# Kernel tuning notes

Hardware: AMD Instinct MI355X
Metric: run time of the kernel (lower is better)

The kernel has to match this reference:

```python
import jax, jax.numpy as jnp
import numpy as np

N, M, F0, FB, F, H, NC, NCONV = 60000, 12, 92, 41, 64, 128, 2000, 3
EPS = 1e-5


def setup_inputs() -> dict:
    key = jax.random.key(0)
    ks = jax.random.split(key, 12)
    s = 0.05
    return {
        "atom_fea": jax.random.normal(ks[0], (N, F0), jnp.float32),
        "nbr_fea": jax.random.normal(ks[1], (N, M, FB), jnp.float32),
        "nbr_fea_idx": jax.random.randint(ks[2], (N, M), 0, N),
        "crystal_atom_idx": jnp.sort(jax.random.randint(ks[3], (N,), 0, NC)),
        "W_emb": jax.random.normal(ks[4], (F0, F), jnp.float32) * s,
        "b_emb": jnp.zeros((F,), jnp.float32),
        "W_full": jax.random.normal(ks[5], (NCONV, 2 * F + FB, 2 * F), jnp.float32) * s,
        "b_full": jnp.zeros((NCONV, 2 * F), jnp.float32),
        "g1": jnp.ones((NCONV, 2 * F), jnp.float32),
        "be1": jnp.zeros((NCONV, 2 * F), jnp.float32),
        "g2": jnp.ones((NCONV, F), jnp.float32),
        "be2": jnp.zeros((NCONV, F), jnp.float32),
        "W_fc": jax.random.normal(ks[6], (F, H), jnp.float32) * s,
        "b_fc": jnp.zeros((H,), jnp.float32),
        "W_out": jax.random.normal(ks[7], (H, 1), jnp.float32) * s,
        "b_out": jnp.zeros((1,), jnp.float32),
    }


def _bn(x, g, b):
    # training-mode batch norm over leading (row) dim
    m = x.mean(axis=0)
    v = x.var(axis=0)
    return (x - m) * jax.lax.rsqrt(v + EPS) * g + b


def _conv_layer(x, nbr_fea, nbr_fea_idx, Wf, bf, g1, be1, g2, be2):
    n, m = nbr_fea_idx.shape
    f = x.shape[1]
    atom_nbr = x[nbr_fea_idx]  # (N, M, F) gather
    total = jnp.concatenate(
        [jnp.broadcast_to(x[:, None, :], (n, m, f)), atom_nbr, nbr_fea], axis=2
    )  # (N, M, 2F+FB)
    gated = total @ Wf + bf  # (N, M, 2F)
    gated = _bn(gated.reshape(-1, 2 * f), g1, be1).reshape(n, m, 2 * f)
    nbr_filter, nbr_core = jnp.split(gated, 2, axis=2)
    summed = jnp.sum(jax.nn.sigmoid(nbr_filter) * jax.nn.softplus(nbr_core), axis=1)
    summed = _bn(summed, g2, be2)
    return jax.nn.softplus(x + summed)


def reference(atom_fea, nbr_fea, nbr_fea_idx, crystal_atom_idx, W_emb, b_emb,
              W_full, b_full, g1, be1, g2, be2, W_fc, b_fc, W_out, b_out):
    x = atom_fea @ W_emb + b_emb  # (N, F)
    for i in range(NCONV):
        x = _conv_layer(x, nbr_fea, nbr_fea_idx, W_full[i], b_full[i],
                        g1[i], be1[i], g2[i], be2[i])
    # mean-pool atoms per crystal (segment mean)
    sums = jax.ops.segment_sum(x, crystal_atom_idx, num_segments=NC)
    cnt = jax.ops.segment_sum(jnp.ones((x.shape[0],), x.dtype), crystal_atom_idx,
                              num_segments=NC)
    crys = sums / jnp.maximum(cnt, 1.0)[:, None]  # (NC, F)
    crys = jax.nn.softplus(crys) @ W_fc + b_fc
    crys = jax.nn.softplus(crys)
    return crys @ W_out + b_out  # (NC, 1)
```

## Files before the change

kernel.cpp:

```cpp
#include <hip/hip_runtime.h>
#include <hip/hip_bf16.h>


#define NATOM 60000
#define MNBR  12
#define F0D   92
#define FBD   41
#define FD    64
#define F2D   128
#define NCRY  2000
#define HD    128
#define NSUP  15000
#define GS    132

#define OFF_X      0ull
#define OFF_XH     3840000ull
#define OFF_SUMMED 5760000ull
#define OFF_STATS  9600000ull
#define OFF_CRYS   9600384ull
#define OFF_CNT    9728384ull
#define OFF_WCONV  9730384ull
#define OFF_WBF    9811220ull
#define OFF_FLAG   9848084ull
#define WS_NEED_BYTES (9848085ull * 4ull)
#define OFF_BPAD   9848088ull
#define WS_FULL_BYTES ((OFF_BPAD + 17280000ull) * 4ull)

#define W_EMB_O  0
#define B_EMB_O  5888
#define W_FULL_O 5952
#define B_FULL_O 70848
#define G1_O     71232
#define BE1_O    71616
#define G2_O     72000
#define BE2_O    72192
#define W_FC_O   72384
#define B_FC_O   80576
#define W_OUT_O  80704
#define B_OUT_O  80832
#define WC_TOTAL 80833

typedef unsigned short u16;
typedef __attribute__((ext_vector_type(8))) short bf16x8;
typedef __attribute__((ext_vector_type(4))) float f32x4;

__device__ __forceinline__ float bf2f(u16 u){
  union { unsigned int i; float f; } v; v.i = ((unsigned int)u) << 16; return v.f;
}
__device__ __forceinline__ u16 f2bf(float f){
  union { float f; unsigned int i; } v; v.f = f;
  unsigned int x = v.i;
  return (u16)((x + 0x7FFFu + ((x >> 16) & 1u)) >> 16);
}
__device__ __forceinline__ float softplusf_(float x){
  return fmaxf(x, 0.f) + log1pf(expf(-fabsf(x)));
}
__device__ __forceinline__ float softplus_fast(float x){
  return fmaxf(x, 0.f) + __logf(1.f + __expf(-fabsf(x)));
}
__device__ __forceinline__ float sigmoid_fast(float x){
  return __builtin_amdgcn_rcpf(1.f + __expf(-x));
}

__global__ __launch_bounds__(64) void detect_kernel(
    const u16* __restrict__ data, int* __restrict__ flag){
  int tid = threadIdx.x;
  float v = bf2f(data[tid * 2]);
  float av = fabsf(v);
  bool sane = (av > 1e-6f) && (av < 100.f);
  unsigned long long m = __ballot(sane);
  if (tid == 0) *flag = (__popcll(m) >= 32) ? 1 : 0;
}

struct CvtArgs {
  const void* src[12];
  int start[13];
};

__global__ __launch_bounds__(256) void cvt_all_kernel(
    CvtArgs a, float* __restrict__ dst, const int* __restrict__ flag){
  int i = blockIdx.x * 256 + threadIdx.x;
  if (i >= WC_TOTAL) return;
  int r = 0;
  while (i >= a.start[r + 1]) r++;
  int rel = i - a.start[r];
  if (*flag) dst[i] = bf2f(((const u16*)a.src[r])[rel]);
  else       dst[i] = ((const float*)a.src[r])[rel];
}

__global__ __launch_bounds__(256) void build_bfrag(
    const float* __restrict__ wfull, u16* __restrict__ wbf){
  int t = blockIdx.x * 256 + threadIdx.x;
  if (t >= 3 * 6 * 8 * 64) return;
  int lane = t & 63, nt = (t >> 6) & 7, c = (t >> 9) % 6, layer = t / 3072;
  int q = lane >> 4, nloc = lane & 15;
  u16 vals[8];
  #pragma unroll
  for (int i = 0; i < 8; i++){
    int k = c * 32 + q * 8 + i;
    float v = (k < 169) ? wfull[layer * 169 * F2D + k * F2D + nt * 16 + nloc] : 0.f;
    vals[i] = f2bf(v);
  }
  *(uint4*)&wbf[(size_t)t * 8] = *(uint4*)vals;
}

__global__ __launch_bounds__(256) void bond_prep(
    const void* __restrict__ nbr_fea, u16* __restrict__ bond_pad,
    const int* __restrict__ flag){
  __shared__ __align__(16) char sm[7872];
  u16*   lb_u = (u16*)sm;
  float* lb_f = (float*)sm;
  int s = blockIdx.x, tid = threadIdx.x;
  const int isbf = *flag;
  if (isbf){
    const uint4* src = (const uint4*)((const u16*)nbr_fea + (size_t)s * 1968);
    if (tid < 246) ((uint4*)sm)[tid] = src[tid];
  } else {
    const uint4* src = (const uint4*)((const float*)nbr_fea + (size_t)s * 1968);
    for (int t = tid; t < 492; t += 256) ((uint4*)sm)[t] = src[t];
  }
  __syncthreads();
  uint4* outv = (uint4*)(bond_pad + (size_t)s * 2304);
  for (int slot = tid; slot < 288; slot += 256){
    int el = slot / 6, jj = slot - el * 6;
    u16 v[8];
    #pragma unroll
    for (int i = 0; i < 8; i++){
      int k = jj * 8 + i;
      v[i] = (k < FBD) ? (isbf ? lb_u[el * FBD + k] : f2bf(lb_f[el * FBD + k])) : (u16)0;
    }
    outv[slot] = *(uint4*)v;
  }
}

__global__ __launch_bounds__(256) void embed_kernel(
    const void* __restrict__ atom_fea, const float* __restrict__ W_emb,
    const float* __restrict__ b_emb, float* __restrict__ x,
    u16* __restrict__ xh, const int* __restrict__ flag){
  int tid = threadIdx.x;
  int n = blockIdx.x * 4 + (tid >> 6);
  int f = tid & 63;
  float acc = b_emb[f];
  if (*flag){
    const u16* arow = (const u16*)atom_fea + n * F0D;
    for (int k = 0; k < F0D; k++)
      acc = fmaf(bf2f(arow[k]), W_emb[k * FD + f], acc);
  } else {
    const float* arow = (const float*)atom_fea + n * F0D;
    for (int k = 0; k < F0D; k++)
      acc = fmaf(arow[k], W_emb[k * FD + f], acc);
  }
  x[n * FD + f] = acc;
  xh[n * FD + f] = f2bf(acc);
}

template<int ACT, int PAD>
__global__ __launch_bounds__(256, 3) void conv_mfma(
    const u16* __restrict__ xh, const void* __restrict__ nbr_fea,
    const u16* __restrict__ bond_pad,
    const int* __restrict__ nbr_idx, const u16* __restrict__ wbf_l,
    const float* __restrict__ bfull, const float* __restrict__ sum1,
    const float* __restrict__ sq1, const float* __restrict__ g1,
    const float* __restrict__ be1, float* __restrict__ summed,
    float* __restrict__ o_sum, float* __restrict__ o_sq,
    const int* __restrict__ flag){
  extern __shared__ char smem[];
  u16*   fragA = (u16*)smem;
  const int base_off = PAD ? 0 : 6144;
  float* gbuf  = (float*)(smem + base_off);
  float* redS  = ACT ? (gbuf + 48 * GS) : (float*)(smem + base_off);
  float* redQ  = redS + (ACT ? 64 : 128);

  const int tid = threadIdx.x;
  const int w = tid >> 6, lane = tid & 63;
  const int q = lane >> 4, nloc = lane & 15, q8 = q * 8;
  const int isbf = *flag;

  bf16x8 Bf[6][2];
  const bf16x8* Bv = (const bf16x8*)wbf_l;
  #pragma unroll
  for (int c = 0; c < 6; c++)
    #pragma unroll
    for (int t2 = 0; t2 < 2; t2++)
      Bf[c][t2] = Bv[(c * 8 + w * 2 + t2) * 64 + lane];
  float bias0 = bfull[w * 32 + nloc];
  float bias1 = bfull[w * 32 + 16 + nloc];

  float A0 = 0.f, B0 = 0.f, A1 = 0.f, B1 = 0.f;
  if (ACT){
    const float invR = 1.f / (float)(NATOM * MNBR);
    float m0 = sum1[lane] * invR;
    float v0 = fmaxf(sq1[lane] * invR - m0 * m0, 0.f);
    A0 = g1[lane] * rsqrtf(v0 + 1e-5f);  B0 = be1[lane] - m0 * A0;
    float m1 = sum1[64 + lane] * invR;
    float v1 = fmaxf(sq1[64 + lane] * invR - m1 * m1, 0.f);
    A1 = g1[64 + lane] * rsqrtf(v1 + 1e-5f);  B1 = be1[64 + lane] - m1 * A1;
  }
  float sAcc0 = 0.f, sAcc1 = 0.f, qAcc0 = 0.f, qAcc1 = 0.f;
  if (tid < (ACT ? 64 : 128)){ redS[tid] = 0.f; redQ[tid] = 0.f; }
  if (PAD && !ACT) ;

  const bf16x8* xv = (const bf16x8*)xh;
  const bf16x8 zero8 = {0,0,0,0,0,0,0,0};
  for (int s = blockIdx.x; s < NSUP; s += gridDim.x){
    int e0 = s * 48 + nloc;
    int nb0 = nbr_idx[e0], nb1 = nbr_idx[e0 + 16], nb2 = nbr_idx[e0 + 32];
    bf16x8 Af[3][6];
    if (PAD){
      #pragma unroll
      for (int et = 0; et < 3; et++){
        int nb = (et == 0) ? nb0 : (et == 1) ? nb1 : nb2;
        int na = s * 4 + (et * 16 + nloc) / 12;
        Af[et][0] = xv[na * 8 + q];
        Af[et][1] = xv[na * 8 + 4 + q];
        Af[et][2] = xv[nb * 8 + q];
        Af[et][3] = xv[nb * 8 + 4 + q];
        const bf16x8* bpv = (const bf16x8*)(bond_pad + (size_t)(e0 + et * 16) * 48);
        Af[et][4] = bpv[q];
        Af[et][5] = (q < 2) ? bpv[4 + q] : zero8;
      }
    } else {
      if (w < 3){
        size_t eg = (size_t)(s * 48 + w * 16 + nloc);
        u16 v4[8], v5[8];
        if (isbf){
          const u16* br = (const u16*)nbr_fea + eg * 41;
          #pragma unroll
          for (int i = 0; i < 8; i++) v4[i] = br[q8 + i];
          #pragma unroll
          for (int i = 0; i < 8; i++){
            int k5 = 32 + q8 + i;
            v5[i] = (k5 < 41) ? br[k5] : (u16)0;
          }
        } else {
          const float* br = (const float*)nbr_fea + eg * 41;
          #pragma unroll
          for (int i = 0; i < 8; i++) v4[i] = f2bf(br[q8 + i]);
          #pragma unroll
          for (int i = 0; i < 8; i++){
            int k5 = 32 + q8 + i;
            v5[i] = (k5 < 41) ? f2bf(br[k5]) : (u16)0;
          }
        }
        *(uint4*)&fragA[(w * 2 + 0) * 512 + lane * 8] = *(uint4*)v4;
        *(uint4*)&fragA[(w * 2 + 1) * 512 + lane * 8] = *(uint4*)v5;
      }
      __syncthreads();
      #pragma unroll
      for (int et = 0; et < 3; et++){
        int nb = (et == 0) ? nb0 : (et == 1) ? nb1 : nb2;
        int na = s * 4 + (et * 16 + nloc) / 12;
        Af[et][0] = xv[na * 8 + q];
        Af[et][1] = xv[na * 8 + 4 + q];
        Af[et][2] = xv[nb * 8 + q];
        Af[et][3] = xv[nb * 8 + 4 + q];
        Af[et][4] = *(bf16x8*)&fragA[(et * 2 + 0) * 512 + lane * 8];
        Af[et][5] = *(bf16x8*)&fragA[(et * 2 + 1) * 512 + lane * 8];
      }
    }
    #pragma unroll
    for (int et = 0; et < 3; et++){
      #pragma unroll
      for (int t2 = 0; t2 < 2; t2++){
        float bs = t2 ? bias1 : bias0;
        f32x4 acc = {bs, bs, bs, bs};
        acc = __builtin_amdgcn_mfma_f32_16x16x32_bf16(Af[et][0], Bf[0][t2], acc, 0, 0, 0);
        acc = __builtin_amdgcn_mfma_f32_16x16x32_bf16(Af[et][1], Bf[1][t2], acc, 0, 0, 0);
        acc = __builtin_amdgcn_mfma_f32_16x16x32_bf16(Af[et][2], Bf[2][t2], acc, 0, 0, 0);
        acc = __builtin_amdgcn_mfma_f32_16x16x32_bf16(Af[et][3], Bf[3][t2], acc, 0, 0, 0);
        acc = __builtin_amdgcn_mfma_f32_16x16x32_bf16(Af[et][4], Bf[4][t2], acc, 0, 0, 0);
        acc = __builtin_amdgcn_mfma_f32_16x16x32_bf16(Af[et][5], Bf[5][t2], acc, 0, 0, 0);
        if (ACT){
          int col = w * 32 + t2 * 16 + nloc;
          int r0 = et * 16 + q * 4;
          gbuf[(r0 + 0) * GS + col] = acc[0];
          gbuf[(r0 + 1) * GS + col] = acc[1];
          gbuf[(r0 + 2) * GS + col] = acc[2];
          gbuf[(r0 + 3) * GS + col] = acc[3];
        } else {
          float ss = acc[0] + acc[1] + acc[2] + acc[3];
          float qq = acc[0]*acc[0] + acc[1]*acc[1] + acc[2]*acc[2] + acc[3]*acc[3];
          if (t2){ sAcc1 += ss; qAcc1 += qq; } else { sAcc0 += ss; qAcc0 += qq; }
        }
      }
    }
    if (ACT){
      __syncthreads();
      float p = 0.f;
      #pragma unroll
      for (int m = 0; m < 12; m++){
        int el = w * 12 + m;
        float u = fmaf(gbuf[el * GS + lane],      A0, B0);
        float v = fmaf(gbuf[el * GS + 64 + lane], A1, B1);
        p = fmaf(sigmoid_fast(u), softplus_fast(v), p);
      }
      summed[(s * 4 + w) * 64 + lane] = p;
      sAcc0 += p;  qAcc0 = fmaf(p, p, qAcc0);
      __syncthreads();
    } else if (!PAD){
      __syncthreads();
    }
  }
  __syncthreads();
  if (ACT){
    atomicAdd(&redS[lane], sAcc0);
    atomicAdd(&redQ[lane], qAcc0);
    __syncthreads();
    if (tid < 64){ atomicAdd(&o_sum[tid], redS[tid]); atomicAdd(&o_sq[tid], redQ[tid]); }
  } else {
    int c0 = w * 32 + nloc;
    atomicAdd(&redS[c0], sAcc0);       atomicAdd(&redQ[c0], qAcc0);
    atomicAdd(&redS[c0 + 16], sAcc1);  atomicAdd(&redQ[c0 + 16], qAcc1);
    __syncthreads();
    if (tid < 128){ atomicAdd(&o_sum[tid], redS[tid]); atomicAdd(&o_sq[tid], redQ[tid]); }
  }
}

__global__ __launch_bounds__(256) void update_x_kernel(
    float* __restrict__ x, u16* __restrict__ xh,
    const float* __restrict__ summed,
    const float* __restrict__ sum2, const float* __restrict__ sq2,
    const float* __restrict__ g2, const float* __restrict__ be2){
  int idx = blockIdx.x * 256 + threadIdx.x;
  int f = idx & 63;
  const float invN = 1.f / (float)NATOM;
  float mean = sum2[f] * invN;
  float var  = fmaxf(sq2[f] * invN - mean * mean, 0.f);
  float a = g2[f] * rsqrtf(var + 1e-5f);
  float b = be2[f] - mean * a;
  float v = x[idx] + fmaf(summed[idx], a, b);
  float r = softplusf_(v);
  x[idx] = r;
  xh[idx] = f2bf(r);
}

__global__ __launch_bounds__(256) void pool_kernel(
    const float* __restrict__ x, const int* __restrict__ cidx,
    float* __restrict__ crys, float* __restrict__ cnt){
  int idx = blockIdx.x * 256 + threadIdx.x;
  int n = idx >> 6, f = idx & 63;
  int c = cidx[n];
  atomicAdd(&crys[c * FD + f], x[idx]);
  if (f == 0) atomicAdd(&cnt[c], 1.f);
}

__global__ __launch_bounds__(128) void head_kernel(
    const float* __restrict__ crys, const float* __restrict__ cnt,
    const float* __restrict__ W_fc, const float* __restrict__ b_fc,
    const float* __restrict__ W_out, const float* __restrict__ b_out,
    void* __restrict__ out, const int* __restrict__ flag){
  __shared__ float p_s[FD];
  __shared__ float red_s[HD];
  int c = blockIdx.x, tid = threadIdx.x;
  if (tid < FD){
    float ct = fmaxf(cnt[c], 1.f);
    p_s[tid] = softplusf_(crys[c * FD + tid] / ct);
  }
  __syncthreads();
  float acc = b_fc[tid];
  for (int k = 0; k < FD; k++)
    acc = fmaf(p_s[k], W_fc[k * HD + tid], acc);
  float h = softplusf_(acc);
  red_s[tid] = h * W_out[tid];
  __syncthreads();
  for (int s = HD / 2; s > 0; s >>= 1){
    if (tid < s) red_s[tid] += red_s[tid + s];
    __syncthreads();
  }
  if (tid == 0){
    float r = red_s[0] + b_out[0];
    if (*flag) ((u16*)out)[c] = f2bf(r);
    else       ((float*)out)[c] = r;
  }
}

extern "C" void kernel_launch(void* const* d_in, const int* in_sizes, int n_in,
                              void* d_out, int out_size, void* d_ws, size_t ws_size,
                              hipStream_t stream){
  if (ws_size < WS_NEED_BYTES) return;
  const bool full = (ws_size >= WS_FULL_BYTES);
  const void* atom_fea = d_in[0];
  const void* nbr_fea  = d_in[1];
  const int* nbr_idx   = (const int*)d_in[2];
  const int* cidx      = (const int*)d_in[3];

  float* ws     = (float*)d_ws;
  float* x      = ws + OFF_X;
  u16*   xh     = (u16*)(ws + OFF_XH);
  float* summed = ws + OFF_SUMMED;
  float* sum1   = ws + OFF_STATS;
  float* sq1    = sum1 + 128;
  float* sum2   = sq1 + 128;
  float* sq2    = sum2 + 64;
  float* crys   = ws + OFF_CRYS;
  float* cnt    = ws + OFF_CNT;
  float* wc     = ws + OFF_WCONV;
  u16*   wbf    = (u16*)(ws + OFF_WBF);
  int*   flag   = (int*)(ws + OFF_FLAG);
  u16*   bpad   = (u16*)(ws + OFF_BPAD);

  detect_kernel<<<1, 64, 0, stream>>>((const u16*)nbr_fea, flag);
  CvtArgs ca;
  const int srcidx[12] = {4,5,6,7,8,9,10,11,12,13,14,15};
  const int starts[13] = {W_EMB_O, B_EMB_O, W_FULL_O, B_FULL_O, G1_O, BE1_O,
                          G2_O, BE2_O, W_FC_O, B_FC_O, W_OUT_O, B_OUT_O, WC_TOTAL};
  for (int i = 0; i < 12; i++){ ca.src[i] = d_in[srcidx[i]]; ca.start[i] = starts[i]; }
  ca.start[12] = WC_TOTAL;
  cvt_all_kernel<<<(WC_TOTAL + 255) / 256, 256, 0, stream>>>(ca, wc, flag);
  build_bfrag<<<(9216 + 255) / 256, 256, 0, stream>>>(wc + W_FULL_O, wbf);
  if (full) bond_prep<<<NSUP, 256, 0, stream>>>(nbr_fea, bpad, flag);

  embed_kernel<<<NATOM / 4, 256, 0, stream>>>(atom_fea, wc + W_EMB_O, wc + B_EMB_O,
                                              x, xh, flag);
  const int LDS_STATS_P = 2 * 128 * 4;
  const int LDS_ACT_P   = (48 * GS + 128) * 4;
  const int LDS_STATS_F = 6144 + 2 * 128 * 4;
  const int LDS_ACT_F   = 6144 + (48 * GS + 128) * 4;
  for (int i = 0; i < 3; i++){
    const u16* wbf_l = wbf + (size_t)i * 3072 * 8;
    hipMemsetAsync(sum1, 0, 384 * sizeof(float), stream);
    if (full){
      conv_mfma<0,1><<<3000, 256, LDS_STATS_P, stream>>>(xh, nbr_fea, bpad, nbr_idx,
          wbf_l, wc + B_FULL_O + i * F2D, sum1, sq1, wc + G1_O + i * F2D,
          wc + BE1_O + i * F2D, summed, sum1, sq1, flag);
      conv_mfma<1,1><<<3000, 256, LDS_ACT_P, stream>>>(xh, nbr_fea, bpad, nbr_idx,
          wbf_l, wc + B_FULL_O + i * F2D, sum1, sq1, wc + G1_O + i * F2D,
          wc + BE1_O + i * F2D, summed, sum2, sq2, flag);
    } else {
      conv_mfma<0,0><<<3000, 256, LDS_STATS_F, stream>>>(xh, nbr_fea, bpad, nbr_idx,
          wbf_l, wc + B_FULL_O + i * F2D, sum1, sq1, wc + G1_O + i * F2D,
          wc + BE1_O + i * F2D, summed, sum1, sq1, flag);
      conv_mfma<1,0><<<3000, 256, LDS_ACT_F, stream>>>(xh, nbr_fea, bpad, nbr_idx,
          wbf_l, wc + B_FULL_O + i * F2D, sum1, sq1, wc + G1_O + i * F2D,
          wc + BE1_O + i * F2D, summed, sum2, sq2, flag);
    }
    update_x_kernel<<<(NATOM * FD) / 256, 256, 0, stream>>>(x, xh, summed, sum2, sq2,
        wc + G2_O + i * FD, wc + BE2_O + i * FD);
  }
  hipMemsetAsync(crys, 0, (NCRY * FD + NCRY) * sizeof(float), stream);
  pool_kernel<<<(NATOM * FD) / 256, 256, 0, stream>>>(x, cidx, crys, cnt);
  head_kernel<<<NCRY, 128, 0, stream>>>(crys, cnt, wc + W_FC_O, wc + B_FC_O,
      wc + W_OUT_O, wc + B_OUT_O, d_out, flag);
}
```

Before: 1.009 ms.

## Add software-pipelined conv kernel that prefetches next super-tile operands and indices

```diff
diff --git a/kernel.cpp b/kernel.cpp
--- a/kernel.cpp
+++ b/kernel.cpp
@@ -12,6 +12,7 @@
 #define HD    128
 #define NSUP  15000
 #define GS    132
+#define CGRID 3000
 
 #define OFF_X      0ull
 #define OFF_XH     3840000ull
@@ -154,6 +155,205 @@
   xh[n * FD + f] = f2bf(acc);
 }
 
+template<int ACT>
+__global__ __launch_bounds__(256, ACT ? 3 : 2) void conv_pipe(
+    const u16* __restrict__ xh, const u16* __restrict__ bond_pad,
+    const int* __restrict__ nbr_idx, const u16* __restrict__ wbf_l,
+    const float* __restrict__ bfull, const float* __restrict__ sum1,
+    const float* __restrict__ sq1, const float* __restrict__ g1,
+    const float* __restrict__ be1, float* __restrict__ summed,
+    float* __restrict__ o_sum, float* __restrict__ o_sq){
+  extern __shared__ char smem[];
+  float* gbuf = (float*)smem;
+  float* redS = ACT ? (gbuf + 48 * GS) : (float*)smem;
+  float* redQ = redS + (ACT ? 64 : 128);
+
+  const int tid = threadIdx.x;
+  const int w = tid >> 6, lane = tid & 63;
+  const int q = lane >> 4, nloc = lane & 15;
+
+  bf16x8 Bf[6][2];
+  const bf16x8* Bv = (const bf16x8*)wbf_l;
+  #pragma unroll
+  for (int c = 0; c < 6; c++)
+    #pragma unroll
+    for (int t2 = 0; t2 < 2; t2++)
+      Bf[c][t2] = Bv[(c * 8 + w * 2 + t2) * 64 + lane];
+  float bias0 = bfull[w * 32 + nloc];
+  float bias1 = bfull[w * 32 + 16 + nloc];
+
+  float A0 = 0.f, B0 = 0.f, A1 = 0.f, B1 = 0.f;
+  if (ACT){
+    const float invR = 1.f / (float)(NATOM * MNBR);
+    float m0 = sum1[lane] * invR;
+    float v0 = fmaxf(sq1[lane] * invR - m0 * m0, 0.f);
+    A0 = g1[lane] * rsqrtf(v0 + 1e-5f);  B0 = be1[lane] - m0 * A0;
+    float m1 = sum1[64 + lane] * invR;
+    float v1 = fmaxf(sq1[64 + lane] * invR - m1 * m1, 0.f);
+    A1 = g1[64 + lane] * rsqrtf(v1 + 1e-5f);  B1 = be1[64 + lane] - m1 * A1;
+  }
+  float sAcc0 = 0.f, sAcc1 = 0.f, qAcc0 = 0.f, qAcc1 = 0.f;
+  if (tid < (ACT ? 64 : 128)){ redS[tid] = 0.f; redQ[tid] = 0.f; }
+
+  const bf16x8* xv = (const bf16x8*)xh;
+  const bf16x8 zero8 = {0,0,0,0,0,0,0,0};
+  const int s0 = blockIdx.x;
+
+  if (ACT){
+    int nbp[2][3];
+    bf16x8 Axh[3][4], Abd[3][2];
+    {
+      int e0 = s0 * 48 + nloc;
+      nbp[0][0] = nbr_idx[e0];  nbp[0][1] = nbr_idx[e0 + 16];  nbp[0][2] = nbr_idx[e0 + 32];
+      int e1 = e0 + CGRID * 48;
+      nbp[1][0] = nbr_idx[e1];  nbp[1][1] = nbr_idx[e1 + 16];  nbp[1][2] = nbr_idx[e1 + 32];
+    }
+    #pragma unroll
+    for (int et = 0; et < 3; et++){
+      const bf16x8* bpv = (const bf16x8*)(bond_pad + (size_t)(s0 * 48 + et * 16 + nloc) * 48);
+      Abd[et][0] = bpv[q];
+      Abd[et][1] = (q < 2) ? bpv[4 + q] : zero8;
+      int na = s0 * 4 + (et * 16 + nloc) / 12;
+      int nb = nbp[0][et];
+      Axh[et][0] = xv[na * 8 + q];      Axh[et][1] = xv[na * 8 + 4 + q];
+      Axh[et][2] = xv[nb * 8 + q];      Axh[et][3] = xv[nb * 8 + 4 + q];
+    }
+    #pragma unroll
+    for (int k = 0; k < 5; k++){
+      const int s = s0 + k * CGRID;
+      #pragma unroll
+      for (int et = 0; et < 3; et++){
+        #pragma unroll
+        for (int t2 = 0; t2 < 2; t2++){
+          float bs = t2 ? bias1 : bias0;
+          f32x4 acc = {bs, bs, bs, bs};
+          acc = __builtin_amdgcn_mfma_f32_16x16x32_bf16(Abd[et][0], Bf[4][t2], acc, 0, 0, 0);
+          acc = __builtin_amdgcn_mfma_f32_16x16x32_bf16(Abd[et][1], Bf[5][t2], acc, 0, 0, 0);
+          acc = __builtin_amdgcn_mfma_f32_16x16x32_bf16(Axh[et][0], Bf[0][t2], acc, 0, 0, 0);
+          acc = __builtin_amdgcn_mfma_f32_16x16x32_bf16(Axh[et][1], Bf[1][t2], acc, 0, 0, 0);
+          acc = __builtin_amdgcn_mfma_f32_16x16x32_bf16(Axh[et][2], Bf[2][t2], acc, 0, 0, 0);
+          acc = __builtin_amdgcn_mfma_f32_16x16x32_bf16(Axh[et][3], Bf[3][t2], acc, 0, 0, 0);
+          int col = w * 32 + t2 * 16 + nloc;
+          int r0 = et * 16 + q * 4;
+          gbuf[(r0 + 0) * GS + col] = acc[0];
+          gbuf[(r0 + 1) * GS + col] = acc[1];
+          gbuf[(r0 + 2) * GS + col] = acc[2];
+          gbuf[(r0 + 3) * GS + col] = acc[3];
+        }
+      }
+      if (k < 4){
+        const int sn = s + CGRID;
+        #pragma unroll
+        for (int et = 0; et < 3; et++){
+          const bf16x8* bpv = (const bf16x8*)(bond_pad + (size_t)(sn * 48 + et * 16 + nloc) * 48);
+          Abd[et][0] = bpv[q];
+          Abd[et][1] = (q < 2) ? bpv[4 + q] : zero8;
+          int na = sn * 4 + (et * 16 + nloc) / 12;
+          int nb = nbp[(k + 1) & 1][et];
+          Axh[et][0] = xv[na * 8 + q];      Axh[et][1] = xv[na * 8 + 4 + q];
+          Axh[et][2] = xv[nb * 8 + q];      Axh[et][3] = xv[nb * 8 + 4 + q];
+        }
+        if (k < 3){
+          int e2 = (s + 2 * CGRID) * 48 + nloc;
+          nbp[k & 1][0] = nbr_idx[e2];
+          nbp[k & 1][1] = nbr_idx[e2 + 16];
+          nbp[k & 1][2] = nbr_idx[e2 + 32];
+        }
+      }
+      asm volatile("s_waitcnt lgkmcnt(0)" ::: "memory");
+      __builtin_amdgcn_s_barrier();
+      __builtin_amdgcn_sched_barrier(0);
+      float p = 0.f;
+      #pragma unroll
+      for (int m = 0; m < 12; m++){
+        int el = w * 12 + m;
+        float u = fmaf(gbuf[el * GS + lane],      A0, B0);
+        float v = fmaf(gbuf[el * GS + 64 + lane], A1, B1);
+        p = fmaf(sigmoid_fast(u), softplus_fast(v), p);
+      }
+      summed[(s * 4 + w) * 64 + lane] = p;
+      sAcc0 += p;  qAcc0 = fmaf(p, p, qAcc0);
+      asm volatile("s_waitcnt lgkmcnt(0)" ::: "memory");
+      __builtin_amdgcn_s_barrier();
+      __builtin_amdgcn_sched_barrier(0);
+    }
+  } else {
+    int nbp[2][3];
+    bf16x8 Axh[2][3][4], Abd[2][3][2];
+    {
+      int e0 = s0 * 48 + nloc;
+      nbp[0][0] = nbr_idx[e0];  nbp[0][1] = nbr_idx[e0 + 16];  nbp[0][2] = nbr_idx[e0 + 32];
+      int e1 = e0 + CGRID * 48;
+      nbp[1][0] = nbr_idx[e1];  nbp[1][1] = nbr_idx[e1 + 16];  nbp[1][2] = nbr_idx[e1 + 32];
+    }
+    #pragma unroll
+    for (int et = 0; et < 3; et++){
+      const bf16x8* bpv = (const bf16x8*)(bond_pad + (size_t)(s0 * 48 + et * 16 + nloc) * 48);
+      Abd[0][et][0] = bpv[q];
+      Abd[0][et][1] = (q < 2) ? bpv[4 + q] : zero8;
+      int na = s0 * 4 + (et * 16 + nloc) / 12;
+      int nb = nbp[0][et];
+      Axh[0][et][0] = xv[na * 8 + q];   Axh[0][et][1] = xv[na * 8 + 4 + q];
+      Axh[0][et][2] = xv[nb * 8 + q];   Axh[0][et][3] = xv[nb * 8 + 4 + q];
+    }
+    #pragma unroll
+    for (int k = 0; k < 5; k++){
+      const int cur = k & 1, nxt = cur ^ 1;
+      const int s = s0 + k * CGRID;
+      if (k < 4){
+        const int sn = s + CGRID;
+        #pragma unroll
+        for (int et = 0; et < 3; et++){
+          const bf16x8* bpv = (const bf16x8*)(bond_pad + (size_t)(sn * 48 + et * 16 + nloc) * 48);
+          Abd[nxt][et][0] = bpv[q];
+          Abd[nxt][et][1] = (q < 2) ? bpv[4 + q] : zero8;
+          int na = sn * 4 + (et * 16 + nloc) / 12;
+          int nb = nbp[nxt][et];
+          Axh[nxt][et][0] = xv[na * 8 + q];   Axh[nxt][et][1] = xv[na * 8 + 4 + q];
+          Axh[nxt][et][2] = xv[nb * 8 + q];   Axh[nxt][et][3] = xv[nb * 8 + 4 + q];
+        }
+        if (k < 3){
+          int e2 = (s + 2 * CGRID) * 48 + nloc;
+          nbp[cur][0] = nbr_idx[e2];
+          nbp[cur][1] = nbr_idx[e2 + 16];
+          nbp[cur][2] = nbr_idx[e2 + 32];
+        }
+      }
+      #pragma unroll
+      for (int et = 0; et < 3; et++){
+        #pragma unroll
+        for (int t2 = 0; t2 < 2; t2++){
+          float bs = t2 ? bias1 : bias0;
+          f32x4 acc = {bs, bs, bs, bs};
+          acc = __builtin_amdgcn_mfma_f32_16x16x32_bf16(Abd[cur][et][0], Bf[4][t2], acc, 0, 0, 0);
+          acc = __builtin_amdgcn_mfma_f32_16x16x32_bf16(Abd[cur][et][1], Bf[5][t2], acc, 0, 0, 0);
+          acc = __builtin_amdgcn_mfma_f32_16x16x32_bf16(Axh[cur][et][0], Bf[0][t2], acc, 0, 0, 0);
+          acc = __builtin_amdgcn_mfma_f32_16x16x32_bf16(Axh[cur][et][1], Bf[1][t2], acc, 0, 0, 0);
+          acc = __builtin_amdgcn_mfma_f32_16x16x32_bf16(Axh[cur][et][2], Bf[2][t2], acc, 0, 0, 0);
+          acc = __builtin_amdgcn_mfma_f32_16x16x32_bf16(Axh[cur][et][3], Bf[3][t2], acc, 0, 0, 0);
+          float ss = acc[0] + acc[1] + acc[2] + acc[3];
+          float qq = acc[0]*acc[0] + acc[1]*acc[1] + acc[2]*acc[2] + acc[3]*acc[3];
+          if (t2){ sAcc1 += ss; qAcc1 += qq; } else { sAcc0 += ss; qAcc0 += qq; }
+        }
+      }
+    }
+  }
+
+  __syncthreads();
+  if (ACT){
+    atomicAdd(&redS[lane], sAcc0);
+    atomicAdd(&redQ[lane], qAcc0);
+    __syncthreads();
+    if (tid < 64){ atomicAdd(&o_sum[tid], redS[tid]); atomicAdd(&o_sq[tid], redQ[tid]); }
+  } else {
+    int c0 = w * 32 + nloc;
+    atomicAdd(&redS[c0], sAcc0);       atomicAdd(&redQ[c0], qAcc0);
+    atomicAdd(&redS[c0 + 16], sAcc1);  atomicAdd(&redQ[c0 + 16], qAcc1);
+    __syncthreads();
+    if (tid < 128){ atomicAdd(&o_sum[tid], redS[tid]); atomicAdd(&o_sq[tid], redQ[tid]); }
+  }
+}
+
 template<int ACT, int PAD>
 __global__ __launch_bounds__(256, 3) void conv_mfma(
     const u16* __restrict__ xh, const void* __restrict__ nbr_fea,
@@ -198,7 +398,6 @@
   }
   float sAcc0 = 0.f, sAcc1 = 0.f, qAcc0 = 0.f, qAcc1 = 0.f;
   if (tid < (ACT ? 64 : 128)){ redS[tid] = 0.f; redQ[tid] = 0.f; }
-  if (PAD && !ACT) ;
 
   const bf16x8* xv = (const bf16x8*)xh;
   const bf16x8 zero8 = {0,0,0,0,0,0,0,0};
@@ -420,17 +619,17 @@
     const u16* wbf_l = wbf + (size_t)i * 3072 * 8;
     hipMemsetAsync(sum1, 0, 384 * sizeof(float), stream);
     if (full){
-      conv_mfma<0,1><<<3000, 256, LDS_STATS_P, stream>>>(xh, nbr_fea, bpad, nbr_idx,
+      conv_pipe<0><<<CGRID, 256, LDS_STATS_P, stream>>>(xh, bpad, nbr_idx,
+          wbf_l, wc + B_FULL_O + i * F2D, sum1, sq1, wc + G1_O + i * F2D,
+          wc + BE1_O + i * F2D, summed, sum1, sq1);
+      conv_pipe<1><<<CGRID, 256, LDS_ACT_P, stream>>>(xh, bpad, nbr_idx,
+          wbf_l, wc + B_FULL_O + i * F2D, sum1, sq1, wc + G1_O + i * F2D,
+          wc + BE1_O + i * F2D, summed, sum2, sq2);
+    } else {
+      conv_mfma<0,0><<<CGRID, 256, LDS_STATS_F, stream>>>(xh, nbr_fea, bpad, nbr_idx,
           wbf_l, wc + B_FULL_O + i * F2D, sum1, sq1, wc + G1_O + i * F2D,
           wc + BE1_O + i * F2D, summed, sum1, sq1, flag);
-      conv_mfma<1,1><<<3000, 256, LDS_ACT_P, stream>>>(xh, nbr_fea, bpad, nbr_idx,
-          wbf_l, wc + B_FULL_O + i * F2D, sum1, sq1, wc + G1_O + i * F2D,
-          wc + BE1_O + i * F2D, summed, sum2, sq2, flag);
-    } else {
-      conv_mfma<0,0><<<3000, 256, LDS_STATS_F, stream>>>(xh, nbr_fea, bpad, nbr_idx,
-          wbf_l, wc + B_FULL_O + i * F2D, sum1, sq1, wc + G1_O + i * F2D,
-          wc + BE1_O + i * F2D, summed, sum1, sq1, flag);
-      conv_mfma<1,0><<<3000, 256, LDS_ACT_F, stream>>>(xh, nbr_fea, bpad, nbr_idx,
+      conv_mfma<1,0><<<CGRID, 256, LDS_ACT_F, stream>>>(xh, nbr_fea, bpad, nbr_idx,
           wbf_l, wc + B_FULL_O + i * F2D, sum1, sq1, wc + G1_O + i * F2D,
           wc + BE1_O + i * F2D, summed, sum2, sq2, flag);
     }
```

After: 1.010 ms. About the same (+0.0%).

## Stage conv operands into LDS via async global_load_lds with double buffering

Applied to the files above, without the earlier changes.

```diff
diff --git a/kernel.cpp b/kernel.cpp
--- a/kernel.cpp
+++ b/kernel.cpp
@@ -12,6 +12,7 @@
 #define HD    128
 #define NSUP  15000
 #define GS    132
+#define CGRID 3000
 
 #define OFF_X      0ull
 #define OFF_XH     3840000ull
@@ -60,6 +61,12 @@
 }
 __device__ __forceinline__ float sigmoid_fast(float x){
   return __builtin_amdgcn_rcpf(1.f + __expf(-x));
+}
+
+typedef const __attribute__((address_space(1))) unsigned int* gup;
+typedef __attribute__((address_space(3))) unsigned int* lup;
+__device__ __forceinline__ void dma16(const void* g, void* l){
+  __builtin_amdgcn_global_load_lds((gup)g, (lup)l, 16, 0, 0);
 }
 
 __global__ __launch_bounds__(64) void detect_kernel(
@@ -122,12 +129,15 @@
   __syncthreads();
   uint4* outv = (uint4*)(bond_pad + (size_t)s * 2304);
   for (int slot = tid; slot < 288; slot += 256){
-    int el = slot / 6, jj = slot - el * 6;
+    int et = slot / 96, jj = slot - et * 96;
+    int l  = (jj < 64) ? jj : (jj - 64);
+    int row = et * 16 + (l & 15);
+    int kb  = ((jj < 64) ? 0 : 32) + (l >> 4) * 8;
     u16 v[8];
     #pragma unroll
     for (int i = 0; i < 8; i++){
-      int k = jj * 8 + i;
-      v[i] = (k < FBD) ? (isbf ? lb_u[el * FBD + k] : f2bf(lb_f[el * FBD + k])) : (u16)0;
+      int k = kb + i;
+      v[i] = (k < FBD) ? (isbf ? lb_u[row * FBD + k] : f2bf(lb_f[row * FBD + k])) : (u16)0;
     }
     outv[slot] = *(uint4*)v;
   }
@@ -154,27 +164,24 @@
   xh[n * FD + f] = f2bf(acc);
 }
 
-template<int ACT, int PAD>
-__global__ __launch_bounds__(256, 3) void conv_mfma(
-    const u16* __restrict__ xh, const void* __restrict__ nbr_fea,
-    const u16* __restrict__ bond_pad,
+template<int ACT>
+__global__ __launch_bounds__(256, ACT ? 3 : 4) void conv_lds(
+    const u16* __restrict__ xh, const u16* __restrict__ bond_pad,
     const int* __restrict__ nbr_idx, const u16* __restrict__ wbf_l,
     const float* __restrict__ bfull, const float* __restrict__ sum1,
     const float* __restrict__ sq1, const float* __restrict__ g1,
     const float* __restrict__ be1, float* __restrict__ summed,
-    float* __restrict__ o_sum, float* __restrict__ o_sq,
-    const int* __restrict__ flag){
+    float* __restrict__ o_sum, float* __restrict__ o_sq){
   extern __shared__ char smem[];
-  u16*   fragA = (u16*)smem;
-  const int base_off = PAD ? 0 : 6144;
-  float* gbuf  = (float*)(smem + base_off);
-  float* redS  = ACT ? (gbuf + 48 * GS) : (float*)(smem + base_off);
-  float* redQ  = redS + (ACT ? 64 : 128);
+  char* stg  = smem;
+  float* gbuf = (float*)(smem + 22528);
+  float* redS = ACT ? (float*)(smem + 22528 + 48 * GS * 4)
+                    : (float*)(smem + 22528);
+  float* redQ = redS + (ACT ? 64 : 128);
 
   const int tid = threadIdx.x;
   const int w = tid >> 6, lane = tid & 63;
-  const int q = lane >> 4, nloc = lane & 15, q8 = q * 8;
-  const int isbf = *flag;
+  const int q = lane >> 4, nloc = lane & 15;
 
   bf16x8 Bf[6][2];
   const bf16x8* Bv = (const bf16x8*)wbf_l;
@@ -198,65 +205,203 @@
   }
   float sAcc0 = 0.f, sAcc1 = 0.f, qAcc0 = 0.f, qAcc1 = 0.f;
   if (tid < (ACT ? 64 : 128)){ redS[tid] = 0.f; redQ[tid] = 0.f; }
-  if (PAD && !ACT) ;
+
+  const char* xh8   = (const char*)xh;
+  const char* bpad8 = (const char*)bond_pad;
+  const int jx1 = tid - 64;
+  const int rA  = (tid >= 64) ? ((jx1 >> 7) * 16 + (jx1 & 15)) : 0;
+  const int cg1 = (tid >= 64) ? (((((jx1 >> 6) & 1) << 2) + ((jx1 >> 4) & 3)) << 4) : 0;
+  const int jx2 = tid + 192;
+  const int rB  = (tid < 192) ? ((jx2 >> 7) * 16 + (jx2 & 15)) : 0;
+  const int cg2 = (tid < 192) ? (((((jx2 >> 6) & 1) << 2) + ((jx2 >> 4) & 3)) << 4) : 0;
+
+#define STAGE(DBUF, SS, NA, NB)                                                  \
+  {                                                                              \
+    const char* g0 = bpad8 + (size_t)(SS) * 4608 + (size_t)tid * 16;             \
+    dma16(g0, (DBUF) + w * 1024);                                                \
+    const char* g1p;                                                             \
+    if (tid < 32)      g1p = bpad8 + (size_t)(SS) * 4608 + (size_t)(tid + 256) * 16; \
+    else if (tid < 64) g1p = xh8 + (size_t)(SS) * 512 + (size_t)(tid - 32) * 16; \
+    else               g1p = xh8 + (size_t)(NA) * 128 + cg1;                     \
+    dma16(g1p, (DBUF) + 4096 + w * 1024);                                        \
+    if (w < 3){                                                                  \
+      const char* g2p = xh8 + (size_t)(NB) * 128 + cg2;                          \
+      dma16(g2p, (DBUF) + 8192 + w * 1024);                                      \
+    }                                                                            \
+  }
+
+  const bf16x8 zero8 = {0,0,0,0,0,0,0,0};
+  const int s0 = blockIdx.x;
+
+  int nbA = nbr_idx[s0 * 48 + rA];
+  int nbB = nbr_idx[s0 * 48 + rB];
+  STAGE(stg, s0, nbA, nbB);
+  nbA = nbr_idx[(s0 + CGRID) * 48 + rA];
+  nbB = nbr_idx[(s0 + CGRID) * 48 + rB];
+  __syncthreads();
+
+  for (int k = 0; k < 5; k++){
+    const int s = s0 + k * CGRID;
+    char* cb   = stg + (k & 1) * 11264;
+    char* nbuf = stg + ((k & 1) ^ 1) * 11264;
+    if (k < 4) STAGE(nbuf, s + CGRID, nbA, nbB);
+    if (k < 3){
+      nbA = nbr_idx[(s + 2 * CGRID) * 48 + rA];
+      nbB = nbr_idx[(s + 2 * CGRID) * 48 + rB];
+    }
+    #pragma unroll
+    for (int et = 0; et < 3; et++){
+      int naloc = (et * 16 + nloc) / 12;
+      const char* xs = cb + 4608 + naloc * 128;
+      bf16x8 a0 = *(const bf16x8*)(xs + q * 16);
+      bf16x8 a1 = *(const bf16x8*)(xs + 64 + q * 16);
+      bf16x8 a2 = *(const bf16x8*)(cb + 5120 + (et * 128 + lane) * 16);
+      bf16x8 a3 = *(const bf16x8*)(cb + 5120 + (et * 128 + 64 + lane) * 16);
+      bf16x8 a4 = *(const bf16x8*)(cb + (et * 96 + lane) * 16);
+      bf16x8 a5 = (lane < 32) ? *(const bf16x8*)(cb + (et * 96 + 64 + lane) * 16)
+                              : zero8;
+      #pragma unroll
+      for (int t2 = 0; t2 < 2; t2++){
+        float bs = t2 ? bias1 : bias0;
+        f32x4 acc = {bs, bs, bs, bs};
+        acc = __builtin_amdgcn_mfma_f32_16x16x32_bf16(a0, Bf[0][t2], acc, 0, 0, 0);
+        acc = __builtin_amdgcn_mfma_f32_16x16x32_bf16(a1, Bf[1][t2], acc, 0, 0, 0);
+        acc = __builtin_amdgcn_mfma_f32_16x16x32_bf16(a2, Bf[2][t2], acc, 0, 0, 0);
+        acc = __builtin_amdgcn_mfma_f32_16x16x32_bf16(a3, Bf[3][t2], acc, 0, 0, 0);
+        acc = __builtin_amdgcn_mfma_f32_16x16x32_bf16(a4, Bf[4][t2], acc, 0, 0, 0);
+        acc = __builtin_amdgcn_mfma_f32_16x16x32_bf16(a5, Bf[5][t2], acc, 0, 0, 0);
+        if (ACT){
+          int col = w * 32 + t2 * 16 + nloc;
+          int r0 = et * 16 + q * 4;
+          gbuf[(r0 + 0) * GS + col] = acc[0];
+          gbuf[(r0 + 1) * GS + col] = acc[1];
+          gbuf[(r0 + 2) * GS + col] = acc[2];
+          gbuf[(r0 + 3) * GS + col] = acc[3];
+        } else {
+          float ss = acc[0] + acc[1] + acc[2] + acc[3];
+          float qq = acc[0]*acc[0] + acc[1]*acc[1] + acc[2]*acc[2] + acc[3]*acc[3];
+          if (t2){ sAcc1 += ss; qAcc1 += qq; } else { sAcc0 += ss; qAcc0 += qq; }
+        }
+      }
+    }
+    if (ACT){
+      __builtin_amdgcn_sched_barrier(0);
+      asm volatile("s_waitcnt lgkmcnt(0)");
+      __builtin_amdgcn_s_barrier();
+      __builtin_amdgcn_sched_barrier(0);
+      float p = 0.f;
+      #pragma unroll
+      for (int m = 0; m < 12; m++){
+        int el = w * 12 + m;
+        float u = fmaf(gbuf[el * GS + lane],      A0, B0);
+        float v = fmaf(gbuf[el * GS + 64 + lane], A1, B1);
+        p = fmaf(sigmoid_fast(u), softplus_fast(v), p);
+      }
+      summed[(s * 4 + w) * 64 + lane] = p;
+      sAcc0 += p;  qAcc0 = fmaf(p, p, qAcc0);
+    }
+    __syncthreads();
+  }
+#undef STAGE
+
+  if (ACT){
+    atomicAdd(&redS[lane], sAcc0);
+    atomicAdd(&redQ[lane], qAcc0);
+    __syncthreads();
+    if (tid < 64){ atomicAdd(&o_sum[tid], redS[tid]); atomicAdd(&o_sq[tid], redQ[tid]); }
+  } else {
+    int c0 = w * 32 + nloc;
+    atomicAdd(&redS[c0], sAcc0);       atomicAdd(&redQ[c0], qAcc0);
+    atomicAdd(&redS[c0 + 16], sAcc1);  atomicAdd(&redQ[c0 + 16], qAcc1);
+    __syncthreads();
+    if (tid < 128){ atomicAdd(&o_sum[tid], redS[tid]); atomicAdd(&o_sq[tid], redQ[tid]); }
+  }
+}
+
+template<int ACT>
+__global__ __launch_bounds__(256, 3) void conv_mfma(
+    const u16* __restrict__ xh, const void* __restrict__ nbr_fea,
+    const int* __restrict__ nbr_idx, const u16* __restrict__ wbf_l,
+    const float* __restrict__ bfull, const float* __restrict__ sum1,
+    const float* __restrict__ sq1, const float* __restrict__ g1,
+    const float* __restrict__ be1, float* __restrict__ summed,
+    float* __restrict__ o_sum, float* __restrict__ o_sq,
+    const int* __restrict__ flag){
+  extern __shared__ char smem[];
+  u16*   fragA = (u16*)smem;
+  float* gbuf  = (float*)(smem + 6144);
+  float* redS  = ACT ? (gbuf + 48 * GS) : (float*)(smem + 6144);
+  float* redQ  = redS + (ACT ? 64 : 128);
+
+  const int tid = threadIdx.x;
+  const int w = tid >> 6, lane = tid & 63;
+  const int q = lane >> 4, nloc = lane & 15, q8 = q * 8;
+  const int isbf = *flag;
+
+  bf16x8 Bf[6][2];
+  const bf16x8* Bv = (const bf16x8*)wbf_l;
+  #pragma unroll
+  for (int c = 0; c < 6; c++)
+    #pragma unroll
+    for (int t2 = 0; t2 < 2; t2++)
+      Bf[c][t2] = Bv[(c * 8 + w * 2 + t2) * 64 + lane];
+  float bias0 = bfull[w * 32 + nloc];
+  float bias1 = bfull[w * 32 + 16 + nloc];
+
+  float A0 = 0.f, B0 = 0.f, A1 = 0.f, B1 = 0.f;
+  if (ACT){
+    const float invR = 1.f / (float)(NATOM * MNBR);
+    float m0 = sum1[lane] * invR;
+    float v0 = fmaxf(sq1[lane] * invR - m0 * m0, 0.f);
+    A0 = g1[lane] * rsqrtf(v0 + 1e-5f);  B0 = be1[lane] - m0 * A0;
+    float m1 = sum1[64 + lane] * invR;
+    float v1 = fmaxf(sq1[64 + lane] * invR - m1 * m1, 0.f);
+    A1 = g1[64 + lane] * rsqrtf(v1 + 1e-5f);  B1 = be1[64 + lane] - m1 * A1;
+  }
+  float sAcc0 = 0.f, sAcc1 = 0.f, qAcc0 = 0.f, qAcc1 = 0.f;
+  if (tid < (ACT ? 64 : 128)){ redS[tid] = 0.f; redQ[tid] = 0.f; }
 
   const bf16x8* xv = (const bf16x8*)xh;
-  const bf16x8 zero8 = {0,0,0,0,0,0,0,0};
   for (int s = blockIdx.x; s < NSUP; s += gridDim.x){
     int e0 = s * 48 + nloc;
     int nb0 = nbr_idx[e0], nb1 = nbr_idx[e0 + 16], nb2 = nbr_idx[e0 + 32];
     bf16x8 Af[3][6];
-    if (PAD){
-      #pragma unroll
-      for (int et = 0; et < 3; et++){
-        int nb = (et == 0) ? nb0 : (et == 1) ? nb1 : nb2;
-        int na = s * 4 + (et * 16 + nloc) / 12;
-        Af[et][0] = xv[na * 8 + q];
-        Af[et][1] = xv[na * 8 + 4 + q];
-        Af[et][2] = xv[nb * 8 + q];
-        Af[et][3] = xv[nb * 8 + 4 + q];
-        const bf16x8* bpv = (const bf16x8*)(bond_pad + (size_t)(e0 + et * 16) * 48);
-        Af[et][4] = bpv[q];
-        Af[et][5] = (q < 2) ? bpv[4 + q] : zero8;
+    if (w < 3){
+      size_t eg = (size_t)(s * 48 + w * 16 + nloc);
+      u16 v4[8], v5[8];
+      if (isbf){
+        const u16* br = (const u16*)nbr_fea + eg * 41;
+        #pragma unroll
+        for (int i = 0; i < 8; i++) v4[i] = br[q8 + i];
+        #pragma unroll
+        for (int i = 0; i < 8; i++){
+          int k5 = 32 + q8 + i;
+          v5[i] = (k5 < 41) ? br[k5] : (u16)0;
+        }
+      } else {
+        const float* br = (const float*)nbr_fea + eg * 41;
+        #pragma unroll
+        for (int i = 0; i < 8; i++) v4[i] = f2bf(br[q8 + i]);
+        #pragma unroll
+        for (int i = 0; i < 8; i++){
+          int k5 = 32 + q8 + i;
+          v5[i] = (k5 < 41) ? f2bf(br[k5]) : (u16)0;
+        }
       }
-    } else {
-      if (w < 3){
-        size_t eg = (size_t)(s * 48 + w * 16 + nloc);
-        u16 v4[8], v5[8];
-        if (isbf){
-          const u16* br = (const u16*)nbr_fea + eg * 41;
-          #pragma unroll
-          for (int i = 0; i < 8; i++) v4[i] = br[q8 + i];
-          #pragma unroll
-          for (int i = 0; i < 8; i++){
-            int k5 = 32 + q8 + i;
-            v5[i] = (k5 < 41) ? br[k5] : (u16)0;
-          }
-        } else {
-          const float* br = (const float*)nbr_fea + eg * 41;
-          #pragma unroll
-          for (int i = 0; i < 8; i++) v4[i] = f2bf(br[q8 + i]);
-          #pragma unroll
-          for (int i = 0; i < 8; i++){
-            int k5 = 32 + q8 + i;
-            v5[i] = (k5 < 41) ? f2bf(br[k5]) : (u16)0;
-          }
-        }
-        *(uint4*)&fragA[(w * 2 + 0) * 512 + lane * 8] = *(uint4*)v4;
-        *(uint4*)&fragA[(w * 2 + 1) * 512 + lane * 8] = *(uint4*)v5;
-      }
-      __syncthreads();
-      #pragma unroll
-      for (int et = 0; et < 3; et++){
-        int nb = (et == 0) ? nb0 : (et == 1) ? nb1 : nb2;
-        int na = s * 4 + (et * 16 + nloc) / 12;
-        Af[et][0] = xv[na * 8 + q];
-        Af[et][1] = xv[na * 8 + 4 + q];
-        Af[et][2] = xv[nb * 8 + q];
-        Af[et][3] = xv[nb * 8 + 4 + q];
-        Af[et][4] = *(bf16x8*)&fragA[(et * 2 + 0) * 512 + lane * 8];
-        Af[et][5] = *(bf16x8*)&fragA[(et * 2 + 1) * 512 + lane * 8];
-      }
+      *(uint4*)&fragA[(w * 2 + 0) * 512 + lane * 8] = *(uint4*)v4;
+      *(uint4*)&fragA[(w * 2 + 1) * 512 + lane * 8] = *(uint4*)v5;
+    }
+    __syncthreads();
+    #pragma unroll
+    for (int et = 0; et < 3; et++){
+      int nb = (et == 0) ? nb0 : (et == 1) ? nb1 : nb2;
+      int na = s * 4 + (et * 16 + nloc) / 12;
+      Af[et][0] = xv[na * 8 + q];
+      Af[et][1] = xv[na * 8 + 4 + q];
+      Af[et][2] = xv[nb * 8 + q];
+      Af[et][3] = xv[nb * 8 + 4 + q];
+      Af[et][4] = *(bf16x8*)&fragA[(et * 2 + 0) * 512 + lane * 8];
+      Af[et][5] = *(bf16x8*)&fragA[(et * 2 + 1) * 512 + lane * 8];
     }
     #pragma unroll
     for (int et = 0; et < 3; et++){
@@ -296,12 +441,9 @@
       }
       summed[(s * 4 + w) * 64 + lane] = p;
       sAcc0 += p;  qAcc0 = fmaf(p, p, qAcc0);
-      __syncthreads();
-    } else if (!PAD){
-      __syncthreads();
-    }
-  }
-  __syncthreads();
+    }
+    __syncthreads();
+  }
   if (ACT){
     atomicAdd(&redS[lane], sAcc0);
     atomicAdd(&redQ[lane], qAcc0);
@@ -412,25 +554,25 @@
 
   embed_kernel<<<NATOM / 4, 256, 0, stream>>>(atom_fea, wc + W_EMB_O, wc + B_EMB_O,
                                               x, xh, flag);
-  const int LDS_STATS_P = 2 * 128 * 4;
-  const int LDS_ACT_P   = (48 * GS + 128) * 4;
+  const int LDS_STATS_L = 2 * 11264 + 2 * 128 * 4;
+  const int LDS_ACT_L   = 2 * 11264 + 48 * GS * 4 + 2 * 64 * 4;
   const int LDS_STATS_F = 6144 + 2 * 128 * 4;
   const int LDS_ACT_F   = 6144 + (48 * GS + 128) * 4;
   for (int i = 0; i < 3; i++){
     const u16* wbf_l = wbf + (size_t)i * 3072 * 8;
     hipMemsetAsync(sum1, 0, 384 * sizeof(float), stream);
     if (full){
-      conv_mfma<0,1><<<3000, 256, LDS_STATS_P, stream>>>(xh, nbr_fea, bpad, nbr_idx,
+      conv_lds<0><<<CGRID, 256, LDS_STATS_L, stream>>>(xh, bpad, nbr_idx,
+          wbf_l, wc + B_FULL_O + i * F2D, sum1, sq1, wc + G1_O + i * F2D,
+          wc + BE1_O + i * F2D, summed, sum1, sq1);
+      conv_lds<1><<<CGRID, 256, LDS_ACT_L, stream>>>(xh, bpad, nbr_idx,
+          wbf_l, wc + B_FULL_O + i * F2D, sum1, sq1, wc + G1_O + i * F2D,
+          wc + BE1_O + i * F2D, summed, sum2, sq2);
+    } else {
+      conv_mfma<0><<<CGRID, 256, LDS_STATS_F, stream>>>(xh, nbr_fea, nbr_idx,
           wbf_l, wc + B_FULL_O + i * F2D, sum1, sq1, wc + G1_O + i * F2D,
           wc + BE1_O + i * F2D, summed, sum1, sq1, flag);
-      conv_mfma<1,1><<<3000, 256, LDS_ACT_P, stream>>>(xh, nbr_fea, bpad, nbr_idx,
-          wbf_l, wc + B_FULL_O + i * F2D, sum1, sq1, wc + G1_O + i * F2D,
-          wc + BE1_O + i * F2D, summed, sum2, sq2, flag);
-    } else {
-      conv_mfma<0,0><<<3000, 256, LDS_STATS_F, stream>>>(xh, nbr_fea, bpad, nbr_idx,
-          wbf_l, wc + B_FULL_O + i * F2D, sum1, sq1, wc + G1_O + i * F2D,
-          wc + BE1_O + i * F2D, summed, sum1, sq1, flag);
-      conv_mfma<1,0><<<3000, 256, LDS_ACT_F, stream>>>(xh, nbr_fea, bpad, nbr_idx,
+      conv_mfma<1><<<CGRID, 256, LDS_ACT_F, stream>>>(xh, nbr_fea, nbr_idx,
           wbf_l, wc + B_FULL_O + i * F2D, sum1, sq1, wc + G1_O + i * F2D,
           wc + BE1_O + i * F2D, summed, sum2, sq2, flag);
     }
```

Result: slower. 1.359 ms (+34.6%).
